# Performance work log

Hardware: AMD Instinct MI355X
Metric: run time of the kernel (lower is better)

The kernel has to match this reference:

```python
import jax, jax.numpy as jnp
import numpy as np

S = 4  # upsample scale


def setup_inputs() -> dict:
    key = jax.random.key(0)
    ks = jax.random.split(key, 8)
    B, C, H, W = 4, 128, 64, 64
    feat_lr = jax.random.normal(ks[0], (B, C, H, W), dtype=jnp.float32)
    # gate: Conv2d(C, C//4, 1, bias=False) -> LeakyReLU(0.2) -> Conv2d(C//4, 1, 1, bias=True) -> Sigmoid
    gate_w1 = jax.random.normal(ks[1], (C, C // 4), dtype=jnp.float32) * 0.05
    gate_w2 = jax.random.normal(ks[2], (C // 4, 1), dtype=jnp.float32) * 0.1
    gate_b2 = jnp.full((1,), -3.0, dtype=jnp.float32)  # init bias per module
    # mlp: Conv2d(C+2, C, 1) -> ReLU -> Conv2d(C, C, 1)
    mlp_w1 = jax.random.normal(ks[3], (C + 2, C), dtype=jnp.float32) * 0.05
    mlp_b1 = jax.random.normal(ks[4], (C,), dtype=jnp.float32) * 0.01
    mlp_w2 = jax.random.normal(ks[5], (C, C), dtype=jnp.float32) * 0.05
    mlp_b2 = jax.random.normal(ks[6], (C,), dtype=jnp.float32) * 0.01
    return {"feat_lr": feat_lr, "gate_w1": gate_w1, "gate_w2": gate_w2,
            "gate_b2": gate_b2, "mlp_w1": mlp_w1, "mlp_b1": mlp_b1,
            "mlp_w2": mlp_w2, "mlp_b2": mlp_b2}


def reference(feat_lr, gate_w1, gate_w2, gate_b2, mlp_w1, mlp_b1, mlp_w2, mlp_b2):
    B, C, H, W = feat_lr.shape
    f = jnp.transpose(feat_lr, (0, 2, 3, 1))  # (B,H,W,C)

    # ---- gate on LR grid (1x1 convs == per-pixel matmuls) ----
    g = f @ gate_w1                              # (B,H,W,C//4)
    g = jnp.where(g >= 0, g, 0.2 * g)            # LeakyReLU(0.2)
    gate = jax.nn.sigmoid(g @ gate_w2 + gate_b2) # (B,H,W,1)

    # ---- subpixel grid: channels [x, y], values in (-1,1) ----
    coords = jnp.linspace(-1.0 + 1.0 / S, 1.0 - 1.0 / S, S, dtype=feat_lr.dtype)
    yy, xx = jnp.meshgrid(coords, coords, indexing="ij")
    grid = jnp.stack([xx, yy], axis=-1)          # (S,S,2)

    # ---- mlp: split first conv weight into feat part and grid part.
    # Since convs are 1x1 and feat_hr is nearest-upsampled (constant over each
    # SxS block) while grid tiles per block, hidden = relu(f@W1f + grid@W1g + b1)
    # broadcast over (block, subpixel) — avoids materializing concat/HR inputs.
    w1_f, w1_g = mlp_w1[:C], mlp_w1[C:]          # (C,C), (2,C)
    h_f = f @ w1_f                               # (B,H,W,C)
    h_g = grid @ w1_g                            # (S,S,C)
    hidden = jax.nn.relu(h_f[:, :, None, :, None, :]
                         + h_g[None, None, :, None, :, :]
                         + mlp_b1)               # (B,H,S,W,S,C)
    res = hidden @ mlp_w2 + mlp_b2               # (B,H,S,W,S,C)

    out = res * gate[:, :, None, :, None, :]     # broadcast gate over block
    out = out.reshape(B, H * S, W * S, C)
    return jnp.transpose(out, (0, 3, 1, 2))      # (B,C,H*S,W*S)
```

## Files before the change

### kernel.cpp

```cpp
#include <hip/hip_runtime.h>
#include <hip/hip_bf16.h>
#include <math.h>


typedef __attribute__((ext_vector_type(8))) short bf16x8;
typedef __attribute__((ext_vector_type(4))) float f32x4;

__device__ inline short f2bf(float v) {
    __hip_bfloat16 b = __float2bfloat16(v);
    return *reinterpret_cast<short*>(&b);
}

__device__ inline void barrier_lgkm() {
    asm volatile("s_waitcnt lgkmcnt(0)" ::: "memory");
    __builtin_amdgcn_s_barrier();
    asm volatile("" ::: "memory");
}

__global__ __launch_bounds__(256) void ipi_pre_kernel(
    const float* __restrict__ w2,
    const float* __restrict__ w1,
    const float* __restrict__ gw1,
    __hip_bfloat16* __restrict__ w2t,
    __hip_bfloat16* __restrict__ w1t_hi,
    __hip_bfloat16* __restrict__ w1t_lo,
    __hip_bfloat16* __restrict__ g1t_hi,
    __hip_bfloat16* __restrict__ g1t_lo)
{
    int gid = blockIdx.x * 256 + threadIdx.x;
    if (gid < 16384) {
        int j = gid >> 7, k = gid & 127;
        w2t[gid] = __float2bfloat16(w2[k * 128 + j]);
    } else if (gid < 32768) {
        int i = gid - 16384, j = i >> 7, c = i & 127;
        float v = w1[c * 128 + j];
        __hip_bfloat16 hi = __float2bfloat16(v);
        w1t_hi[i] = hi;
        w1t_lo[i] = __float2bfloat16(v - __bfloat162float(hi));
    } else if (gid < 36864) {
        int i = gid - 32768, jg = i >> 7, c = i & 127;
        float v = gw1[c * 32 + jg];
        __hip_bfloat16 hi = __float2bfloat16(v);
        g1t_hi[i] = hi;
        g1t_lo[i] = __float2bfloat16(v - __bfloat162float(hi));
    }
}

__global__ __launch_bounds__(256, 4) void ipi_main(
    const float* __restrict__ feat,
    const float* __restrict__ mlp_w1,
    const float* __restrict__ mlp_b1,
    const float* __restrict__ gate_w2,
    const float* __restrict__ gate_b2,
    const float* __restrict__ mlp_b2,
    const __hip_bfloat16* __restrict__ w2t,
    const __hip_bfloat16* __restrict__ w1t_hi,
    const __hip_bfloat16* __restrict__ w1t_lo,
    const __hip_bfloat16* __restrict__ g1t_hi,
    const __hip_bfloat16* __restrict__ g1t_lo,
    float* __restrict__ out)
{
    __shared__ float hf_s[16 * 132];
    __shared__ float hgb_s[16 * 132];
    __shared__ float gate_s[16];
    __shared__ char  hid[16384];
    short* f_hi = (short*)hid;
    short* f_lo = (short*)(hid + 4352);
    float* glds = (float*)(hid + 8704);

    const int t    = threadIdx.x;
    const int lane = t & 63;
    const int lg   = lane >> 4;
    const int ml   = lane & 15;
    const int wv   = t >> 6;
    const int bx   = blockIdx.x;
    const int w0   = (bx & 3) * 16;
    const int h    = (bx >> 2) & 63;
    const int b    = bx >> 8;

    bf16x8 wfrag[2][4];
    f32x4  b2s[2];
    {
        const __hip_bfloat16* base = w2t + (wv * 32 + ml) * 128 + lg * 8;
        #pragma unroll
        for (int jt = 0; jt < 2; ++jt) {
            #pragma unroll
            for (int ks = 0; ks < 4; ++ks)
                wfrag[jt][ks] = *(const bf16x8*)(base + jt * 2048 + ks * 32);
            float bj = mlp_b2[wv * 32 + jt * 16 + ml];
            b2s[jt] = (f32x4){bj, bj, bj, bj};
        }
    }

    float* pq = out + ((size_t)(b * 128 + wv * 32 + ml) << 16)
                    + (size_t)(h * 4) * 256 + w0 * 4 + lg * 4;

    {
        const float* fbase = feat + ((size_t)(b * 128) * 64 + h) * 64 + w0;
        #pragma unroll
        for (int i = 0; i < 8; ++i) {
            int idx = t + i * 256;
            int c = idx >> 4, w = idx & 15;
            float v = fbase[(size_t)c * 4096 + w];
            short hi = f2bf(v);
            float hf32 = __bfloat162float(*(__hip_bfloat16*)&hi);
            f_hi[w * 136 + c] = hi;
            f_lo[w * 136 + c] = f2bf(v - hf32);
        }
        #pragma unroll
        for (int i = 0; i < 8; ++i) {
            int idx = t + i * 256;
            int s = idx >> 7, k = idx & 127;
            float cx = -0.75f + 0.5f * (float)(s & 3);
            float cy = -0.75f + 0.5f * (float)(s >> 2);
            hgb_s[s * 132 + k] = cx * mlp_w1[16384 + k]
                               + cy * mlp_w1[16512 + k] + mlp_b1[k];
        }
    }
    barrier_lgkm();

    {
        bf16x8 fhi[4], flo[4];
        {
            const short* fb  = f_hi + ml * 136 + lg * 8;
            const short* flb = f_lo + ml * 136 + lg * 8;
            #pragma unroll
            for (int ks = 0; ks < 4; ++ks) {
                fhi[ks] = *(const bf16x8*)(fb + ks * 32);
                flo[ks] = *(const bf16x8*)(flb + ks * 32);
            }
        }
        #pragma unroll
        for (int jj = 0; jj < 2; ++jj) {
            const int jt16 = (wv * 2 + jj) * 16;
            const __hip_bfloat16* bh = w1t_hi + (jt16 + ml) * 128 + lg * 8;
            const __hip_bfloat16* bl = w1t_lo + (jt16 + ml) * 128 + lg * 8;
            f32x4 acc = {0.f, 0.f, 0.f, 0.f};
            #pragma unroll
            for (int ks = 0; ks < 4; ++ks) {
                bf16x8 Bh = *(const bf16x8*)(bh + ks * 32);
                bf16x8 Bl = *(const bf16x8*)(bl + ks * 32);
                acc = __builtin_amdgcn_mfma_f32_16x16x32_bf16(fhi[ks], Bh, acc, 0, 0, 0);
                acc = __builtin_amdgcn_mfma_f32_16x16x32_bf16(fhi[ks], Bl, acc, 0, 0, 0);
                acc = __builtin_amdgcn_mfma_f32_16x16x32_bf16(flo[ks], Bh, acc, 0, 0, 0);
            }
            #pragma unroll
            for (int r = 0; r < 4; ++r)
                hf_s[(lg * 4 + r) * 132 + jt16 + ml] = acc[r];
        }
        if (wv == 0) {
            #pragma unroll
            for (int jt = 0; jt < 2; ++jt) {
                const __hip_bfloat16* bh = g1t_hi + (jt * 16 + ml) * 128 + lg * 8;
                const __hip_bfloat16* bl = g1t_lo + (jt * 16 + ml) * 128 + lg * 8;
                f32x4 acc = {0.f, 0.f, 0.f, 0.f};
                #pragma unroll
                for (int ks = 0; ks < 4; ++ks) {
                    bf16x8 Bh = *(const bf16x8*)(bh + ks * 32);
                    bf16x8 Bl = *(const bf16x8*)(bl + ks * 32);
                    acc = __builtin_amdgcn_mfma_f32_16x16x32_bf16(fhi[ks], Bh, acc, 0, 0, 0);
                    acc = __builtin_amdgcn_mfma_f32_16x16x32_bf16(fhi[ks], Bl, acc, 0, 0, 0);
                    acc = __builtin_amdgcn_mfma_f32_16x16x32_bf16(flo[ks], Bh, acc, 0, 0, 0);
                }
                #pragma unroll
                for (int r = 0; r < 4; ++r) {
                    float v = acc[r];
                    glds[(lg * 4 + r) * 33 + jt * 16 + ml] = (v >= 0.f) ? v : 0.2f * v;
                }
            }
        }
    }
    barrier_lgkm();

    if (t < 16) {
        float s = gate_b2[0];
        #pragma unroll 8
        for (int jg = 0; jg < 32; ++jg) s = fmaf(glds[t * 33 + jg], gate_w2[jg], s);
        gate_s[t] = 1.f / (1.f + expf(-s));
    }
    barrier_lgkm();

    const int mq  = t >> 3;
    const int kq  = t & 7;
    for (int q = 0; q < 4; ++q) {
        {
            const int m0 = t >> 2;
            const int w  = m0 >> 2;
            const int s  = (q << 2) | (m0 & 3);
            const float* hfr = hf_s  + w * 132 + (t & 3) * 32;
            const float* hgr = hgb_s + s * 132 + (t & 3) * 32;
            char* wp = hid + (m0 & 31) * 256 + (m0 >> 5) * 8192;
            const int sw = (m0 & 7) << 4;
            const int kb = (t & 3) * 64;
            #pragma unroll
            for (int kc = 0; kc < 4; ++kc) {
                float4 a0 = *(const float4*)(hfr + kc * 8);
                float4 a1 = *(const float4*)(hfr + kc * 8 + 4);
                float4 g0 = *(const float4*)(hgr + kc * 8);
                float4 g1 = *(const float4*)(hgr + kc * 8 + 4);
                bf16x8 hv;
                hv[0] = f2bf(fmaxf(a0.x + g0.x, 0.f));
                hv[1] = f2bf(fmaxf(a0.y + g0.y, 0.f));
                hv[2] = f2bf(fmaxf(a0.z + g0.z, 0.f));
                hv[3] = f2bf(fmaxf(a0.w + g0.w, 0.f));
                hv[4] = f2bf(fmaxf(a1.x + g1.x, 0.f));
                hv[5] = f2bf(fmaxf(a1.y + g1.y, 0.f));
                hv[6] = f2bf(fmaxf(a1.z + g1.z, 0.f));
                hv[7] = f2bf(fmaxf(a1.w + g1.w, 0.f));
                *(bf16x8*)(wp + ((kb + kc * 16) ^ sw)) = hv;
            }
        }
        barrier_lgkm();

        #pragma unroll
        for (int mt = 0; mt < 4; ++mt) {
            const int mrow = mt * 16 + ml;
            const int swb  = ((mrow & 7) << 4);
            const char* rp = hid + (mrow & 31) * 256 + (mrow >> 5) * 8192;
            bf16x8 hfrag[4];
            #pragma unroll
            for (int ks = 0; ks < 4; ++ks)
                hfrag[ks] = *(const bf16x8*)(rp + ((ks * 64 + lg * 16) ^ swb));

            const float g = gate_s[mt * 4 + lg];

            #pragma unroll
            for (int jt = 0; jt < 2; ++jt) {
                f32x4 acc = b2s[jt];
                #pragma unroll
                for (int ks = 0; ks < 4; ++ks)
                    acc = __builtin_amdgcn_mfma_f32_16x16x32_bf16(hfrag[ks], wfrag[jt][ks], acc, 0, 0, 0);
                float4 o;
                o.x = acc[0] * g; o.y = acc[1] * g;
                o.z = acc[2] * g; o.w = acc[3] * g;
                *(float4*)(pq + ((size_t)(jt * 16) << 16) + q * 256 + mt * 16) = o;
            }
        }
        barrier_lgkm();
    }
    (void)mq; (void)kq;
}

extern "C" void kernel_launch(void* const* d_in, const int* in_sizes, int n_in,
                              void* d_out, int out_size, void* d_ws, size_t ws_size,
                              hipStream_t stream) {
    const float* feat = (const float*)d_in[0];
    const float* gw1  = (const float*)d_in[1];
    const float* gw2  = (const float*)d_in[2];
    const float* gb2  = (const float*)d_in[3];
    const float* w1   = (const float*)d_in[4];
    const float* b1   = (const float*)d_in[5];
    const float* w2   = (const float*)d_in[6];
    const float* b2   = (const float*)d_in[7];
    float* o = (float*)d_out;

    char* ws = (char*)d_ws;
    __hip_bfloat16* w2t    = (__hip_bfloat16*)(ws);
    __hip_bfloat16* w1t_hi = (__hip_bfloat16*)(ws + 32768);
    __hip_bfloat16* w1t_lo = (__hip_bfloat16*)(ws + 65536);
    __hip_bfloat16* g1t_hi = (__hip_bfloat16*)(ws + 98304);
    __hip_bfloat16* g1t_lo = (__hip_bfloat16*)(ws + 106496);

    ipi_pre_kernel<<<dim3(144), dim3(256), 0, stream>>>(
        w2, w1, gw1, w2t, w1t_hi, w1t_lo, g1t_hi, g1t_lo);
    ipi_main<<<dim3(1024), dim3(256), 0, stream>>>(
        feat, w1, b1, gw2, gb2, b2, w2t, w1t_hi, w1t_lo, g1t_hi, g1t_lo, o);
}
```

Baseline: 44.97 us.

## Build MFMA hidden fragments in registers instead of staging through LDS

Each lane now forms its own bf16 hidden-activation A fragments directly from hf_s and hgb_s (add, ReLU, convert) and feeds them straight into the MFMAs. This removes the intermediate swizzled LDS hidden buffer and the two barriers per q iteration. The shared buffers are split into separate arrays, and gate values are hoisted into registers. The trade-off is redundant ReLU and convert work across the two output tiles' source reads and more LDS float reads per lane, in exchange for fewer barriers and less LDS write traffic.

```diff
diff --git a/kernel.cpp b/kernel.cpp
--- a/kernel.cpp
+++ b/kernel.cpp
@@ -63,10 +63,9 @@
     __shared__ float hf_s[16 * 132];
     __shared__ float hgb_s[16 * 132];
     __shared__ float gate_s[16];
-    __shared__ char  hid[16384];
-    short* f_hi = (short*)hid;
-    short* f_lo = (short*)(hid + 4352);
-    float* glds = (float*)(hid + 8704);
+    __shared__ short f_hi[16 * 136];
+    __shared__ short f_lo[16 * 136];
+    __shared__ float glds[16 * 33];
 
     const int t    = threadIdx.x;
     const int lane = t & 63;
@@ -180,65 +179,54 @@
     }
     barrier_lgkm();
 
-    const int mq  = t >> 3;
-    const int kq  = t & 7;
+    const int sx   = ml & 3;
+    const int wrow = ml >> 2;
+    float gq[4];
+    #pragma unroll
+    for (int mt = 0; mt < 4; ++mt) gq[mt] = gate_s[mt * 4 + lg];
+
+    #pragma unroll 1
     for (int q = 0; q < 4; ++q) {
-        {
-            const int m0 = t >> 2;
-            const int w  = m0 >> 2;
-            const int s  = (q << 2) | (m0 & 3);
-            const float* hfr = hf_s  + w * 132 + (t & 3) * 32;
-            const float* hgr = hgb_s + s * 132 + (t & 3) * 32;
-            char* wp = hid + (m0 & 31) * 256 + (m0 >> 5) * 8192;
-            const int sw = (m0 & 7) << 4;
-            const int kb = (t & 3) * 64;
-            #pragma unroll
-            for (int kc = 0; kc < 4; ++kc) {
-                float4 a0 = *(const float4*)(hfr + kc * 8);
-                float4 a1 = *(const float4*)(hfr + kc * 8 + 4);
-                float4 g0 = *(const float4*)(hgr + kc * 8);
-                float4 g1 = *(const float4*)(hgr + kc * 8 + 4);
-                bf16x8 hv;
-                hv[0] = f2bf(fmaxf(a0.x + g0.x, 0.f));
-                hv[1] = f2bf(fmaxf(a0.y + g0.y, 0.f));
-                hv[2] = f2bf(fmaxf(a0.z + g0.z, 0.f));
-                hv[3] = f2bf(fmaxf(a0.w + g0.w, 0.f));
-                hv[4] = f2bf(fmaxf(a1.x + g1.x, 0.f));
-                hv[5] = f2bf(fmaxf(a1.y + g1.y, 0.f));
-                hv[6] = f2bf(fmaxf(a1.z + g1.z, 0.f));
-                hv[7] = f2bf(fmaxf(a1.w + g1.w, 0.f));
-                *(bf16x8*)(wp + ((kb + kc * 16) ^ sw)) = hv;
-            }
-        }
-        barrier_lgkm();
+        const float* hgr = hgb_s + (q * 4 + sx) * 132 + lg * 8;
+        float4 hg0[4], hg1[4];
+        #pragma unroll
+        for (int ks = 0; ks < 4; ++ks) {
+            hg0[ks] = *(const float4*)(hgr + ks * 32);
+            hg1[ks] = *(const float4*)(hgr + ks * 32 + 4);
+        }
 
         #pragma unroll
         for (int mt = 0; mt < 4; ++mt) {
-            const int mrow = mt * 16 + ml;
-            const int swb  = ((mrow & 7) << 4);
-            const char* rp = hid + (mrow & 31) * 256 + (mrow >> 5) * 8192;
-            bf16x8 hfrag[4];
-            #pragma unroll
-            for (int ks = 0; ks < 4; ++ks)
-                hfrag[ks] = *(const bf16x8*)(rp + ((ks * 64 + lg * 16) ^ swb));
-
-            const float g = gate_s[mt * 4 + lg];
-
-            #pragma unroll
-            for (int jt = 0; jt < 2; ++jt) {
-                f32x4 acc = b2s[jt];
-                #pragma unroll
-                for (int ks = 0; ks < 4; ++ks)
-                    acc = __builtin_amdgcn_mfma_f32_16x16x32_bf16(hfrag[ks], wfrag[jt][ks], acc, 0, 0, 0);
-                float4 o;
-                o.x = acc[0] * g; o.y = acc[1] * g;
-                o.z = acc[2] * g; o.w = acc[3] * g;
-                *(float4*)(pq + ((size_t)(jt * 16) << 16) + q * 256 + mt * 16) = o;
-            }
-        }
-        barrier_lgkm();
-    }
-    (void)mq; (void)kq;
+            const float* hfr = hf_s + (mt * 4 + wrow) * 132 + lg * 8;
+            f32x4 acc0 = b2s[0];
+            f32x4 acc1 = b2s[1];
+            #pragma unroll
+            for (int ks = 0; ks < 4; ++ks) {
+                float4 a0 = *(const float4*)(hfr + ks * 32);
+                float4 a1 = *(const float4*)(hfr + ks * 32 + 4);
+                bf16x8 bf;
+                bf[0] = f2bf(fmaxf(a0.x + hg0[ks].x, 0.f));
+                bf[1] = f2bf(fmaxf(a0.y + hg0[ks].y, 0.f));
+                bf[2] = f2bf(fmaxf(a0.z + hg0[ks].z, 0.f));
+                bf[3] = f2bf(fmaxf(a0.w + hg0[ks].w, 0.f));
+                bf[4] = f2bf(fmaxf(a1.x + hg1[ks].x, 0.f));
+                bf[5] = f2bf(fmaxf(a1.y + hg1[ks].y, 0.f));
+                bf[6] = f2bf(fmaxf(a1.z + hg1[ks].z, 0.f));
+                bf[7] = f2bf(fmaxf(a1.w + hg1[ks].w, 0.f));
+                acc0 = __builtin_amdgcn_mfma_f32_16x16x32_bf16(bf, wfrag[0][ks], acc0, 0, 0, 0);
+                acc1 = __builtin_amdgcn_mfma_f32_16x16x32_bf16(bf, wfrag[1][ks], acc1, 0, 0, 0);
+            }
+
+            const float g = gq[mt];
+            float4 o;
+            o.x = acc0[0] * g; o.y = acc0[1] * g;
+            o.z = acc0[2] * g; o.w = acc0[3] * g;
+            *(float4*)(pq + q * 256 + mt * 16) = o;
+            o.x = acc1[0] * g; o.y = acc1[1] * g;
+            o.z = acc1[2] * g; o.w = acc1[3] * g;
+            *(float4*)(pq + ((size_t)16 << 16) + q * 256 + mt * 16) = o;
+        }
+    }
 }
 
 extern "C" void kernel_launch(void* const* d_in, const int* in_sizes, int n_in,
```

New measurement: 125.9 us. 180% more time.

## Switch second MLP matmul to 32x32x16 MFMA with transposed output mapping

Applied to the files above, without the earlier changes.

Replaces the 16x16x32 bf16 MFMA tiles in the hidden@W2 stage with 32x32x16 MFMA, swapping operand roles so weights are the A operand and hidden pixels the B operand. The hidden LDS layout drops its two-half split, and output stores become per-lane scalar writes where consecutive lanes hit consecutive pixels, giving coalesced 128B rows instead of float4 stores across channels. This uses fewer MFMA and LDS-read instructions per output but holds more accumulator and bias registers, which may lower occupancy.

```diff
diff --git a/kernel.cpp b/kernel.cpp
--- a/kernel.cpp
+++ b/kernel.cpp
@@ -5,6 +5,7 @@
 
 typedef __attribute__((ext_vector_type(8))) short bf16x8;
 typedef __attribute__((ext_vector_type(4))) float f32x4;
+typedef __attribute__((ext_vector_type(16))) float f32x16;
 
 __device__ inline short f2bf(float v) {
     __hip_bfloat16 b = __float2bfloat16(v);
@@ -72,28 +73,28 @@
     const int lane = t & 63;
     const int lg   = lane >> 4;
     const int ml   = lane & 15;
+    const int l32  = lane & 31;
+    const int lh   = lane >> 5;
     const int wv   = t >> 6;
     const int bx   = blockIdx.x;
     const int w0   = (bx & 3) * 16;
     const int h    = (bx >> 2) & 63;
     const int b    = bx >> 8;
 
-    bf16x8 wfrag[2][4];
-    f32x4  b2s[2];
+    bf16x8 wfrag[8];
     {
-        const __hip_bfloat16* base = w2t + (wv * 32 + ml) * 128 + lg * 8;
-        #pragma unroll
-        for (int jt = 0; jt < 2; ++jt) {
-            #pragma unroll
-            for (int ks = 0; ks < 4; ++ks)
-                wfrag[jt][ks] = *(const bf16x8*)(base + jt * 2048 + ks * 32);
-            float bj = mlp_b2[wv * 32 + jt * 16 + ml];
-            b2s[jt] = (f32x4){bj, bj, bj, bj};
-        }
-    }
-
-    float* pq = out + ((size_t)(b * 128 + wv * 32 + ml) << 16)
-                    + (size_t)(h * 4) * 256 + w0 * 4 + lg * 4;
+        const __hip_bfloat16* base = w2t + (wv * 32 + l32) * 128 + lh * 8;
+        #pragma unroll
+        for (int ks = 0; ks < 8; ++ks)
+            wfrag[ks] = *(const bf16x8*)(base + ks * 16);
+    }
+    float b2v[16];
+    #pragma unroll
+    for (int r = 0; r < 16; ++r)
+        b2v[r] = mlp_b2[wv * 32 + (r & 3) + 8 * (r >> 2) + 4 * lh];
+
+    float* pq = out + ((size_t)(b * 128 + wv * 32 + 4 * lh) << 16)
+                    + (size_t)(h * 4) * 256 + w0 * 4 + l32;
 
     {
         const float* fbase = feat + ((size_t)(b * 128) * 64 + h) * 64 + w0;
@@ -180,8 +181,6 @@
     }
     barrier_lgkm();
 
-    const int mq  = t >> 3;
-    const int kq  = t & 7;
     for (int q = 0; q < 4; ++q) {
         {
             const int m0 = t >> 2;
@@ -189,7 +188,7 @@
             const int s  = (q << 2) | (m0 & 3);
             const float* hfr = hf_s  + w * 132 + (t & 3) * 32;
             const float* hgr = hgb_s + s * 132 + (t & 3) * 32;
-            char* wp = hid + (m0 & 31) * 256 + (m0 >> 5) * 8192;
+            char* wp = hid + m0 * 256;
             const int sw = (m0 & 7) << 4;
             const int kb = (t & 3) * 64;
             #pragma unroll
@@ -213,32 +212,32 @@
         barrier_lgkm();
 
         #pragma unroll
-        for (int mt = 0; mt < 4; ++mt) {
-            const int mrow = mt * 16 + ml;
-            const int swb  = ((mrow & 7) << 4);
-            const char* rp = hid + (mrow & 31) * 256 + (mrow >> 5) * 8192;
-            bf16x8 hfrag[4];
-            #pragma unroll
-            for (int ks = 0; ks < 4; ++ks)
-                hfrag[ks] = *(const bf16x8*)(rp + ((ks * 64 + lg * 16) ^ swb));
-
-            const float g = gate_s[mt * 4 + lg];
-
-            #pragma unroll
-            for (int jt = 0; jt < 2; ++jt) {
-                f32x4 acc = b2s[jt];
-                #pragma unroll
-                for (int ks = 0; ks < 4; ++ks)
-                    acc = __builtin_amdgcn_mfma_f32_16x16x32_bf16(hfrag[ks], wfrag[jt][ks], acc, 0, 0, 0);
-                float4 o;
-                o.x = acc[0] * g; o.y = acc[1] * g;
-                o.z = acc[2] * g; o.w = acc[3] * g;
-                *(float4*)(pq + ((size_t)(jt * 16) << 16) + q * 256 + mt * 16) = o;
+        for (int mt = 0; mt < 2; ++mt) {
+            const int m  = mt * 32 + l32;
+            const char* rp = hid + m * 256;
+            const int swb = (m & 7) << 4;
+            bf16x8 hfrag[8];
+            #pragma unroll
+            for (int ks = 0; ks < 8; ++ks)
+                hfrag[ks] = *(const bf16x8*)(rp + ((ks * 32 + lh * 16) ^ swb));
+
+            f32x16 acc;
+            #pragma unroll
+            for (int r = 0; r < 16; ++r) acc[r] = b2v[r];
+            #pragma unroll
+            for (int ks = 0; ks < 8; ++ks)
+                acc = __builtin_amdgcn_mfma_f32_32x32x16_bf16(wfrag[ks], hfrag[ks], acc, 0, 0, 0);
+
+            const float g = gate_s[mt * 8 + (l32 >> 2)];
+            float* op = pq + q * 256 + mt * 32;
+            #pragma unroll
+            for (int r = 0; r < 16; ++r) {
+                const size_t joff = (size_t)((r & 3) + 8 * (r >> 2)) << 16;
+                op[joff] = acc[r] * g;
             }
         }
         barrier_lgkm();
     }
-    (void)mq; (void)kq;
 }
 
 extern "C" void kernel_launch(void* const* d_in, const int* in_sizes, int n_in,
```

New measurement: 46.02 us. 2.3% more time.
